# Kernel tuning notes

Measured on AMD Instinct MI355X. Metric: run time of the kernel, lower is better.

Reference implementation:

```python
import jax, jax.numpy as jnp
import numpy as np

B, N, D = 2, 4096, 256
H = 8
HD = D // H  # head dim = 32
DFF = 4 * D


def _layer_norm(x):
    # Matches source: (x - mean) / (std + 1e-6), std is population std (ddof=0)
    m = jnp.mean(x, axis=-1, keepdims=True)
    s = jnp.std(x, axis=-1, keepdims=True)
    return (x - m) / (s + 1e-6)


def setup_inputs() -> dict:
    key = jax.random.key(0)
    ks = jax.random.split(key, 11)
    sd = 1.0 / np.sqrt(D)
    sf = 1.0 / np.sqrt(DFF)
    return {
        "embeddings_in": jax.random.normal(ks[0], (B, N, D), dtype=jnp.float32),
        "Wq": jax.random.normal(ks[1], (D, D), dtype=jnp.float32) * sd,
        "bq": jnp.zeros((D,), dtype=jnp.float32),
        "Wk": jax.random.normal(ks[2], (D, D), dtype=jnp.float32) * sd,
        "bk": jnp.zeros((D,), dtype=jnp.float32),
        "Wv": jax.random.normal(ks[3], (D, D), dtype=jnp.float32) * sd,
        "bv": jnp.zeros((D,), dtype=jnp.float32),
        "Wo": jax.random.normal(ks[4], (D, D), dtype=jnp.float32) * sd,
        "bo": jnp.zeros((D,), dtype=jnp.float32),
        "W1": jax.random.normal(ks[5], (D, DFF), dtype=jnp.float32) * sd,
        "b1": jnp.zeros((DFF,), dtype=jnp.float32),
        "W2": jax.random.normal(ks[6], (DFF, D), dtype=jnp.float32) * sf,
        "b2": jnp.zeros((D,), dtype=jnp.float32),
    }


def reference(embeddings_in, Wq, bq, Wk, bk, Wv, bv, Wo, bo, W1, b1, W2, b2):
    x = embeddings_in
    xn1 = _layer_norm(x)
    # QKV projections, split into heads: [B,N,D] -> [B,H,N,HD]
    def heads(t):
        return jnp.transpose(t.reshape(B, N, H, HD), (0, 2, 1, 3))
    q = heads(xn1 @ Wq + bq)
    k = heads(xn1 @ Wk + bk)
    v = heads(xn1 @ Wv + bv)
    scores = jnp.einsum('bhnd,bhmd->bhnm', q, k) / jnp.sqrt(jnp.float32(HD))
    attn = jax.nn.softmax(scores, axis=-1)
    heads_out = jnp.einsum('bhnm,bhmd->bhnd', attn, v)
    attn_out = jnp.transpose(heads_out, (0, 2, 1, 3)).reshape(B, N, D)
    attn_out = attn_out @ Wo + bo  # dropout is identity in eval
    x_skip = attn_out + x
    xn2 = _layer_norm(x_skip)
    mlp = jax.nn.gelu(xn2 @ W1 + b1) @ W2 + b2
    return mlp + x_skip
```

## Files before the change

### kernel.cpp

```cpp
#include <hip/hip_runtime.h>
#include <hip/hip_bf16.h>

#define Bb 2
#define Nn 4096
#define Dd 256
#define Hh 8
#define HDh 32
#define DFFd 1024
#define MT (Bb*Nn)
#define Tt ((size_t)MT * Dd)
#define SPLIT 4
#define KVB (Nn / SPLIT)
#define NSTP (KVB / 64)

typedef __attribute__((ext_vector_type(8))) short short8;
typedef __attribute__((ext_vector_type(4))) float f32x4;
typedef __attribute__((address_space(1))) const unsigned int gu32;
typedef __attribute__((address_space(3))) unsigned int lu32;

__device__ __forceinline__ void gll16(const ushort* g, ushort* l) {
  __builtin_amdgcn_global_load_lds((gu32*)g, (lu32*)l, 16, 0, 0);
}
__device__ __forceinline__ float bf2f(ushort u){
  union { unsigned int i; float f; } v; v.i = ((unsigned int)u) << 16; return v.f;
}
__device__ __forceinline__ ushort f2bf(float f){
  union { float f; unsigned int i; } v; v.f = f;
  unsigned int r = v.i + 0x7fffu + ((v.i >> 16) & 1u);
  return (ushort)(r >> 16);
}
__device__ __forceinline__ int ars(int r){ return r * 64 + (r >> 3) * 32; }
__device__ __forceinline__ float gelu_f(float c){
  const float u = c * c;
  const float s = __builtin_fmaf(0.044715f * u, c, c);
  const float m = __builtin_amdgcn_exp2f(-2.302144404f * s);
  return c * __builtin_amdgcn_rcpf(1.0f + m);
}

__device__ __forceinline__ void ln_rows4(const float* __restrict__ x,
                                         ushort* __restrict__ out, int row0,
                                         int wave, int lane)
{
  #pragma unroll
  for (int r = 0; r < 4; r++) {
    const int row = row0 + wave * 4 + r;
    const float4 u = *(const float4*)(x + (size_t)row * Dd + lane * 4);
    float s1 = u.x + u.y + u.z + u.w;
    float s2 = u.x*u.x + u.y*u.y + u.z*u.z + u.w*u.w;
    #pragma unroll
    for (int m = 1; m < 64; m <<= 1) { s1 += __shfl_xor(s1, m, 64); s2 += __shfl_xor(s2, m, 64); }
    const float mean = s1 * (1.0f / Dd);
    float var = s2 * (1.0f / Dd) - mean * mean;
    var = var < 0.f ? 0.f : var;
    const float inv = 1.0f / (sqrtf(var) + 1e-6f);
    ushort4 o;
    o.x = f2bf((u.x - mean) * inv); o.y = f2bf((u.y - mean) * inv);
    o.z = f2bf((u.z - mean) * inv); o.w = f2bf((u.w - mean) * inv);
    *(ushort4*)(out + (size_t)row * Dd + lane * 4) = o;
  }
}

__global__ __launch_bounds__(256) void p0_kernel(
    const float* __restrict__ Wq, const float* __restrict__ Wk,
    const float* __restrict__ Wv, const float* __restrict__ Wo,
    const float* __restrict__ W1, const float* __restrict__ W2,
    const float* __restrict__ bq, const float* __restrict__ bk,
    const float* __restrict__ bv, ushort* __restrict__ wt,
    float* __restrict__ bqkv, const float* __restrict__ x,
    ushort* __restrict__ xn1)
{
  const int bid = blockIdx.x, t = threadIdx.x;
  __shared__ __align__(16) ushort T[64][72];
  if (bid < 192) {
    const float* src; ushort* dst; int Nsrc, Kdst, kt, nt;
    if (bid < 64) {
      const int m = bid >> 4, tile = bid & 15;
      kt = tile >> 2; nt = tile & 3; Nsrc = 256; Kdst = 256;
      src = (m == 0 ? Wq : m == 1 ? Wk : m == 2 ? Wv : Wo);
      dst = (m == 3) ? (wt + 196608) : (wt + m * 65536);
    } else if (bid < 128) {
      const int tile = bid - 64; kt = tile >> 4; nt = tile & 15;
      Nsrc = 1024; Kdst = 256; src = W1; dst = wt + 262144;
    } else {
      const int tile = bid - 128; kt = tile >> 2; nt = tile & 3;
      Nsrc = 256; Kdst = 1024; src = W2; dst = wt + 524288;
    }
    const int k0 = kt * 64, n0 = nt * 64;
    const int cc = t & 15, rr = t >> 4;
    #pragma unroll
    for (int pass = 0; pass < 4; pass++) {
      const int k = rr + pass * 16;
      const float4 v = *(const float4*)(src + (size_t)(k0 + k) * Nsrc + n0 + cc * 4);
      T[cc * 4 + 0][k] = f2bf(v.x); T[cc * 4 + 1][k] = f2bf(v.y);
      T[cc * 4 + 2][k] = f2bf(v.z); T[cc * 4 + 3][k] = f2bf(v.w);
    }
    __syncthreads();
    const int nl = t >> 2, ks = (t & 3) * 16;
    const short8 a = *(const short8*)(&T[nl][ks]);
    const short8 b = *(const short8*)(&T[nl][ks + 8]);
    ushort* drow = dst + (size_t)(n0 + nl) * Kdst + k0 + ks;
    *(short8*)(drow) = a; *(short8*)(drow + 8) = b;
  } else if (bid == 192) {
    bqkv[t] = bq[t]; bqkv[256 + t] = bk[t]; bqkv[512 + t] = bv[t];
  }
  ln_rows4(x, xn1, bid * 16, t >> 6, t & 63);
}

__global__ __launch_bounds__(256) void ln_kernel(const float* __restrict__ x,
                                                 ushort* __restrict__ out)
{
  ln_rows4(x, out, blockIdx.x * 16, threadIdx.x >> 6, threadIdx.x & 63);
}

template<int EPI>
__global__ __launch_bounds__(256) void gemm_wide(
    const ushort* __restrict__ A, const ushort* __restrict__ BT,
    const float* __restrict__ bias, void* __restrict__ outv, int N, int K)
{
  __shared__ __align__(16) ushort As[2][128 * 64];
  __shared__ __align__(16) ushort Bs[2][128 * 64];
  const int tid = threadIdx.x;
  const int wave = tid >> 6, lane = tid & 63;
  const int quad = lane >> 4, l15 = lane & 15;
  const int wm = wave >> 1, wn = wave & 1;
  const int n0 = blockIdx.x * 128, m0 = blockIdx.y * 128;
  f32x4 acc[4][4];
  #pragma unroll
  for (int mt = 0; mt < 4; mt++)
    #pragma unroll
    for (int nt = 0; nt < 4; nt++) acc[mt][nt] = (f32x4){0.f,0.f,0.f,0.f};
  const int srow = lane >> 3, scol = ((lane & 7) ^ srow) * 8;
  const ushort* gA[4];
  const ushort* gB[4];
  #pragma unroll
  for (int i = 0; i < 4; i++) {
    gA[i] = A  + (size_t)(m0 + i * 32 + wave * 8 + srow) * K + scol;
    gB[i] = BT + (size_t)(n0 + i * 32 + wave * 8 + srow) * K + scol;
  }
  int aoff[4], boff[4], cx[2];
  #pragma unroll
  for (int mt = 0; mt < 4; mt++) aoff[mt] = (wm * 64 + mt * 16 + l15) * 64;
  #pragma unroll
  for (int nt = 0; nt < 4; nt++) boff[nt] = (wn * 64 + nt * 16 + l15) * 64;
  #pragma unroll
  for (int kk = 0; kk < 2; kk++) cx[kk] = ((kk * 4 + quad) ^ (l15 & 7)) * 8;
  #pragma unroll
  for (int i = 0; i < 4; i++) {
    gll16(gA[i], &As[0][(i * 32 + wave * 8) * 64]);
    gll16(gB[i], &Bs[0][(i * 32 + wave * 8) * 64]);
  }
  __syncthreads();
  const int NC = K >> 6;
  int p = 0;
  for (int c = 0; c < NC; c++) {
    if (c + 1 < NC) {
      #pragma unroll
      for (int i = 0; i < 4; i++) {
        gll16(gA[i] + (c + 1) * 64, &As[p ^ 1][(i * 32 + wave * 8) * 64]);
        gll16(gB[i] + (c + 1) * 64, &Bs[p ^ 1][(i * 32 + wave * 8) * 64]);
      }
    }
    #pragma unroll
    for (int kk = 0; kk < 2; kk++) {
      short8 af[4];
      #pragma unroll
      for (int mt = 0; mt < 4; mt++)
        af[mt] = *(const short8*)(&As[p][aoff[mt] + cx[kk]]);
      #pragma unroll
      for (int nt = 0; nt < 4; nt++) {
        const short8 bf = *(const short8*)(&Bs[p][boff[nt] + cx[kk]]);
        #pragma unroll
        for (int mt = 0; mt < 4; mt++)
          acc[mt][nt] = __builtin_amdgcn_mfma_f32_16x16x32_bf16(af[mt], bf, acc[mt][nt], 0, 0, 0);
      }
    }
    __syncthreads();
    p ^= 1;
  }
  #pragma unroll
  for (int mt = 0; mt < 4; mt++) {
    const int row0 = m0 + wm * 64 + mt * 16 + quad * 4;
    #pragma unroll
    for (int nt = 0; nt < 4; nt++) {
      const int col = n0 + wn * 64 + nt * 16 + l15;
      const float bv = bias[col];
      float c[4];
      #pragma unroll
      for (int i = 0; i < 4; i++) c[i] = acc[mt][nt][i] + bv;
      if (EPI == 0) {
        ushort* qkv = (ushort*)outv;
        const int w = col >> 8, cd = col & 255;
        const int h = cd >> 5, hd = cd & 31;
        const int b = row0 >> 12, n = row0 & (Nn - 1);
        if (w < 2) {
          const float sc2 = (w == 0) ? (1.4426950408889634f * 0.17677669529663687f) : 1.0f;
          ushort* dst = qkv + (size_t)w * Tt + ((size_t)((b * Hh + h) * Nn) + n) * HDh + hd;
          #pragma unroll
          for (int i = 0; i < 4; i++) dst[(size_t)i * HDh] = f2bf(c[i] * sc2);
        } else {
          ushort4 pk;
          pk.x = f2bf(c[0]); pk.y = f2bf(c[1]); pk.z = f2bf(c[2]); pk.w = f2bf(c[3]);
          *(ushort4*)(qkv + 2 * Tt + ((size_t)((b * Hh + h) * HDh + hd)) * Nn + n) = pk;
        }
      } else {
        ushort* out = (ushort*)outv;
        #pragma unroll
        for (int i = 0; i < 4; i++)
          out[(size_t)(row0 + i) * N + col] = f2bf(gelu_f(c[i]));
      }
    }
  }
}

template<int EPI, int BM>
__global__ __launch_bounds__(256) void gemm_epi(
    const ushort* __restrict__ A, const ushort* __restrict__ BT,
    const float* __restrict__ bias, const float* __restrict__ res,
    void* __restrict__ outv, int N, int K)
{
  constexpr int MI = BM / 64;
  constexpr int AI = BM / 32;
  __shared__ __align__(16) ushort AsF[2][BM * 64 + (BM / 8) * 32];
  __shared__ __align__(16) ushort BsF[2][64 * 64 + 8 * 32];
  const int tid = threadIdx.x;
  const int wave = tid >> 6, lane = tid & 63;
  const int quad = lane >> 4, l15 = lane & 15;
  const int n0 = blockIdx.x * 64, m0 = blockIdx.y * BM;
  f32x4 acc[MI][4];
  #pragma unroll
  for (int mt = 0; mt < MI; mt++)
    #pragma unroll
    for (int nt = 0; nt < 4; nt++) acc[mt][nt] = (f32x4){0.f,0.f,0.f,0.f};
  const int srow = lane >> 3, scol = ((lane & 7) ^ srow) * 8;
  const ushort* gA[AI];
  #pragma unroll
  for (int ai = 0; ai < AI; ai++)
    gA[ai] = A + (size_t)(m0 + ai * 32 + wave * 8 + srow) * K + scol;
  const ushort* gB[2];
  #pragma unroll
  for (int bi = 0; bi < 2; bi++)
    gB[bi] = BT + (size_t)(n0 + bi * 32 + wave * 8 + srow) * K + scol;
  int aoff[MI], boff[4];
  #pragma unroll
  for (int mt = 0; mt < MI; mt++) aoff[mt] = ars(wave * 16 * MI + mt * 16 + l15);
  #pragma unroll
  for (int nt = 0; nt < 4; nt++) boff[nt] = ars(nt * 16 + l15);
  int cx[2];
  #pragma unroll
  for (int kk = 0; kk < 2; kk++) cx[kk] = ((kk * 4 + quad) ^ (l15 & 7)) * 8;
  #pragma unroll
  for (int ai = 0; ai < AI; ai++) gll16(gA[ai], &AsF[0][ars(ai * 32 + wave * 8)]);
  #pragma unroll
  for (int bi = 0; bi < 2; bi++) gll16(gB[bi], &BsF[0][ars(bi * 32 + wave * 8)]);
  __syncthreads();
  const int NC = K >> 6;
  int p = 0;
  for (int c = 0; c < NC; c++) {
    if (c + 1 < NC) {
      #pragma unroll
      for (int ai = 0; ai < AI; ai++)
        gll16(gA[ai] + (c + 1) * 64, &AsF[p ^ 1][ars(ai * 32 + wave * 8)]);
      #pragma unroll
      for (int bi = 0; bi < 2; bi++)
        gll16(gB[bi] + (c + 1) * 64, &BsF[p ^ 1][ars(bi * 32 + wave * 8)]);
    }
    #pragma unroll
    for (int kk = 0; kk < 2; kk++) {
      short8 af[MI];
      #pragma unroll
      for (int mt = 0; mt < MI; mt++)
        af[mt] = *(const short8*)(&AsF[p][aoff[mt] + cx[kk]]);
      #pragma unroll
      for (int nt = 0; nt < 4; nt++) {
        const short8 bf = *(const short8*)(&BsF[p][boff[nt] + cx[kk]]);
        #pragma unroll
        for (int mt = 0; mt < MI; mt++)
          acc[mt][nt] = __builtin_amdgcn_mfma_f32_16x16x32_bf16(af[mt], bf, acc[mt][nt], 0, 0, 0);
      }
    }
    __syncthreads();
    p ^= 1;
  }
  #pragma unroll
  for (int mt = 0; mt < MI; mt++) {
    const int row0 = m0 + wave * (16 * MI) + mt * 16 + quad * 4;
    #pragma unroll
    for (int nt = 0; nt < 4; nt++) {
      const int col = n0 + nt * 16 + l15;
      const float bv = bias[col];
      float c[4];
      #pragma unroll
      for (int i = 0; i < 4; i++) c[i] = acc[mt][nt][i] + bv;
      if (EPI == 1) {
        float* out = (float*)outv;
        #pragma unroll
        for (int i = 0; i < 4; i++) {
          const size_t idx = (size_t)(row0 + i) * N + col;
          out[idx] = c[i] + res[idx];
        }
      } else {
        ushort* out = (ushort*)outv;
        #pragma unroll
        for (int i = 0; i < 4; i++)
          out[(size_t)(row0 + i) * N + col] = f2bf(gelu_f(c[i]));
      }
    }
  }
}

__global__ __launch_bounds__(256, 4) void attn_kernel(
    const ushort* __restrict__ qp, const ushort* __restrict__ kp,
    const ushort* __restrict__ vtg, ushort* __restrict__ op0,
    ushort* __restrict__ op123, float* __restrict__ lp)
{
  __shared__ __align__(16) ushort Ks[2][64][32];
  __shared__ __align__(16) ushort Vt[2][32][72];
  __shared__ __align__(16) ushort Ps[4][64][40];
  const int tid = threadIdx.x;
  const int wave = tid >> 6, lane = tid & 63;
  const int quad = lane >> 4, l15 = lane & 15;
  const int qtb = blockIdx.x, bh = blockIdx.y, sp = blockIdx.z;
  const size_t base = (size_t)bh * Nn * HDh;
  const int q0 = qtb * 256 + wave * 64;
  short8 qf[4];
  #pragma unroll
  for (int qt = 0; qt < 4; qt++)
    qf[qt] = *(const short8*)(qp + base + (size_t)(q0 + qt * 16 + l15) * HDh + quad * 8);
  const int kv0 = sp * KVB;
  const ushort* kg = kp + base + (size_t)(kv0 + wave * 16 + (lane >> 2)) * HDh
                   + (((lane & 3) ^ ((lane >> 3) & 3)) * 8);
  const int kc = (quad ^ ((l15 >> 1) & 3)) * 8;
  const int vr = tid >> 3, vc = (tid & 7) * 8;
  const ushort* vg = vtg + base + (size_t)vr * Nn + kv0 + vc;
  ushort* psw = &Ps[wave][0][0];
  f32x4 o[2][4], ol[4];
  #pragma unroll
  for (int qt = 0; qt < 4; qt++) {
    o[0][qt] = (f32x4){0,0,0,0}; o[1][qt] = (f32x4){0,0,0,0};
    ol[qt] = (f32x4){0,0,0,0};
  }
  const short one = (short)0x3F80;
  const short8 ones = {one,one,one,one,one,one,one,one};
  const f32x4 zero4 = {0,0,0,0};
  const float SA = 8388608.0f;
  const float SB = 1065102389.0f;
  gll16(kg, &Ks[0][wave * 16][0]);
  int4 vreg = *(const int4*)vg;
  *(int4*)(&Vt[0][vr][vc]) = vreg;
  vreg = *(const int4*)(vg + 64);
  __syncthreads();
  #pragma unroll 2
  for (int step = 0; step < NSTP; step++) {
    const int p = step & 1;
    if (step + 1 < NSTP) {
      gll16(kg + (size_t)(step + 1) * 64 * HDh, &Ks[p ^ 1][wave * 16][0]);
      *(int4*)(&Vt[p ^ 1][vr][vc]) = vreg;
    }
    if (step + 2 < NSTP) vreg = *(const int4*)(vg + (size_t)(step + 2) * 64);
    #pragma unroll
    for (int half = 0; half < 2; half++) {
      #pragma unroll
      for (int nt2 = 0; nt2 < 2; nt2++) {
        const int nt = half * 2 + nt2;
        const short8 kf = *(const short8*)(&Ks[p][nt * 16 + l15][kc]);
        #pragma unroll
        for (int qt = 0; qt < 4; qt++) {
          const f32x4 s = __builtin_amdgcn_mfma_f32_16x16x32_bf16(kf, qf[qt], zero4, 0, 0, 0);
          const unsigned int i0 = (unsigned int)(int)fmaf(s[0], SA, SB);
          const unsigned int i1 = (unsigned int)(int)fmaf(s[1], SA, SB);
          const unsigned int i2 = (unsigned int)(int)fmaf(s[2], SA, SB);
          const unsigned int i3 = (unsigned int)(int)fmaf(s[3], SA, SB);
          uint2 pk;
          pk.x = __builtin_amdgcn_perm(i1, i0, 0x07060302u);
          pk.y = __builtin_amdgcn_perm(i3, i2, 0x07060302u);
          *(uint2*)(psw + (qt * 16 + l15) * 40 + nt2 * 16 + quad * 4) = pk;
        }
      }
      __builtin_amdgcn_wave_barrier();
      const short8 v0 = *(const short8*)(&Vt[p][l15][half * 32 + quad * 8]);
      const short8 v1 = *(const short8*)(&Vt[p][16 + l15][half * 32 + quad * 8]);
      #pragma unroll
      for (int qt = 0; qt < 4; qt++) {
        const short8 pb = *(const short8*)(psw + (qt * 16 + l15) * 40 + quad * 8);
        o[0][qt] = __builtin_amdgcn_mfma_f32_16x16x32_bf16(v0, pb, o[0][qt], 0, 0, 0);
        o[1][qt] = __builtin_amdgcn_mfma_f32_16x16x32_bf16(v1, pb, o[1][qt], 0, 0, 0);
        ol[qt]   = __builtin_amdgcn_mfma_f32_16x16x32_bf16(ones, pb, ol[qt], 0, 0, 0);
      }
      __builtin_amdgcn_wave_barrier();
    }
    __syncthreads();
  }
  lp[(size_t)sp * (16 * Nn) + (size_t)bh * Nn + q0 + lane] = ol[lane >> 4][0];
  ushort* ob = (sp == 0 ? op0 : op123 + (size_t)(sp - 1) * (16 * (size_t)Nn * HDh));
  #pragma unroll
  for (int pass = 0; pass < 2; pass++) {
    #pragma unroll
    for (int qt2 = 0; qt2 < 2; qt2++) {
      const int qt = pass * 2 + qt2;
      #pragma unroll
      for (int dt = 0; dt < 2; dt++) {
        ushort4 pk;
        pk.x = f2bf(o[dt][qt][0]); pk.y = f2bf(o[dt][qt][1]);
        pk.z = f2bf(o[dt][qt][2]); pk.w = f2bf(o[dt][qt][3]);
        *(ushort4*)(psw + (qt2 * 16 + l15) * 40 + dt * 16 + quad * 4) = pk;
      }
    }
    __builtin_amdgcn_wave_barrier();
    #pragma unroll
    for (int j = 0; j < 2; j++) {
      const int row = j * 16 + (lane >> 2);
      const short8 ov = *(const short8*)(psw + row * 40 + (lane & 3) * 8);
      const int q = q0 + pass * 32 + row;
      *(short8*)(ob + ((size_t)bh * Nn + q) * HDh + (lane & 3) * 8) = ov;
    }
    __builtin_amdgcn_wave_barrier();
  }
}

__global__ __launch_bounds__(256) void attn_combine(
    const ushort* __restrict__ op0, const ushort* __restrict__ op123,
    const float* __restrict__ lp, ushort* __restrict__ attn)
{
  const int idx = blockIdx.x * 256 + threadIdx.x;
  const int d8 = idx & 3, n = (idx >> 2) & (Nn - 1), bh = idx >> 14;
  const size_t ln = (size_t)bh * Nn + n;
  float l = 0.f;
  #pragma unroll
  for (int sp = 0; sp < SPLIT; sp++) l += lp[(size_t)sp * (16 * Nn) + ln];
  const float inv = 1.0f / l;
  float acc[8];
  #pragma unroll
  for (int k = 0; k < 8; k++) acc[k] = 0.f;
  const size_t qoff = ln * HDh + d8 * 8;
  #pragma unroll
  for (int sp = 0; sp < SPLIT; sp++) {
    const ushort* src = (sp == 0 ? op0 : op123 + (size_t)(sp - 1) * (16 * (size_t)Nn * HDh)) + qoff;
    const short8 u = *(const short8*)src;
    #pragma unroll
    for (int k = 0; k < 8; k++) acc[k] += bf2f((ushort)u[k]);
  }
  short8 ov;
  #pragma unroll
  for (int k = 0; k < 8; k++) ov[k] = (short)f2bf(acc[k] * inv);
  const int b = bh >> 3, h = bh & 7;
  *(short8*)(attn + ((size_t)(b * Nn + n)) * Dd + h * HDh + d8 * 8) = ov;
}

extern "C" void kernel_launch(void* const* d_in, const int* in_sizes, int n_in,
                              void* d_out, int out_size, void* d_ws, size_t ws_size,
                              hipStream_t stream)
{
  const float* x  = (const float*)d_in[0];
  const float* Wq = (const float*)d_in[1];
  const float* bq = (const float*)d_in[2];
  const float* Wk = (const float*)d_in[3];
  const float* bk = (const float*)d_in[4];
  const float* Wv = (const float*)d_in[5];
  const float* bv = (const float*)d_in[6];
  const float* Wo = (const float*)d_in[7];
  const float* bo = (const float*)d_in[8];
  const float* W1 = (const float*)d_in[9];
  const float* b1 = (const float*)d_in[10];
  const float* W2 = (const float*)d_in[11];
  const float* b2 = (const float*)d_in[12];

  char* ws = (char*)d_ws;
  ushort* wt    = (ushort*)ws;
  ushort* wtqkv = wt;
  ushort* wto   = wt + 196608;
  ushort* wt1   = wt + 262144;
  ushort* wt2   = wt + 524288;
  float*  bqkv  = (float*)(ws + 786432 * 2);
  ushort* s0    = (ushort*)(ws + 786432 * 2 + 4096);
  ushort* s1    = s0 + Tt;
  ushort* s2    = s1 + Tt;
  ushort* s3    = s2 + Tt;
  float*  xsk   = (float*)(s3 + Tt);
  ushort* xn2   = (ushort*)(xsk + Tt);
  ushort* xn1   = s0;
  ushort* hid   = s0;
  ushort* op0   = s0;
  ushort* op123 = (ushort*)xsk;
  float*  lp    = (float*)d_out;
  ushort* attnb = (ushort*)((char*)d_out + (4u << 20));
  float*  outp  = (float*)d_out;

  const dim3 blk(256);
  hipLaunchKernelGGL(p0_kernel, dim3(512), blk, 0, stream,
                     Wq, Wk, Wv, Wo, W1, W2, bq, bk, bv, wt, bqkv, x, xn1);
  hipLaunchKernelGGL((gemm_wide<0>), dim3(6, 64), blk, 0, stream,
                     xn1, wtqkv, bqkv, (void*)s1, 768, Dd);

  hipLaunchKernelGGL(attn_kernel, dim3(Nn / 256, Bb * Hh, SPLIT), blk, 0, stream,
                     s1, s2, s3, op0, op123, lp);
  hipLaunchKernelGGL(attn_combine, dim3((Bb * Hh * Nn * 4) / 256), blk, 0, stream,
                     op0, op123, lp, attnb);

  hipLaunchKernelGGL((gemm_epi<1,64>), dim3(4, 128), blk, 0, stream,
                     attnb, wto, bo, x, (void*)xsk, Dd, Dd);
  hipLaunchKernelGGL(ln_kernel, dim3(MT / 16), blk, 0, stream, xsk, xn2);
  hipLaunchKernelGGL((gemm_wide<2>), dim3(8, 64), blk, 0, stream,
                     xn2, wt1, b1, (void*)hid, DFFd, Dd);
  hipLaunchKernelGGL((gemm_epi<1,128>), dim3(4, 64), blk, 0, stream,
                     hid, wt2, b2, xsk, (void*)outp, Dd, DFFd);
}
```

Before: 189.4 us.

## Fuse attention split-combine, output projection, residual and LayerNorm into one kernel

Replaces the attn_combine, Wo GEMM and ln_kernel launches with a single wo_ln kernel. It merges the split-KV partial outputs while staging A tiles, runs the 256-wide Wo GEMM per 32-row block, and adds bias and the residual. It then computes the row LayerNorm in-register via shuffles and shared memory. This removes two launches and the round-trips of the combined attention tensor and xsk through global memory. The workspace is remapped so the hidden activation is split across two buffers, which needs extra pointer selection in the MLP GEMMs. The cost is a small per-block tile (grid of 256 blocks) with full Wo staged per block, which may reduce GEMM efficiency.

Measured after the change: 184.6 us. 1.03x faster.

```diff
diff --git a/kernel.cpp b/kernel.cpp
--- a/kernel.cpp
+++ b/kernel.cpp
@@ -106,16 +106,11 @@
   ln_rows4(x, xn1, bid * 16, t >> 6, t & 63);
 }
 
-__global__ __launch_bounds__(256) void ln_kernel(const float* __restrict__ x,
-                                                 ushort* __restrict__ out)
-{
-  ln_rows4(x, out, blockIdx.x * 16, threadIdx.x >> 6, threadIdx.x & 63);
-}
-
 template<int EPI>
 __global__ __launch_bounds__(256) void gemm_wide(
     const ushort* __restrict__ A, const ushort* __restrict__ BT,
-    const float* __restrict__ bias, void* __restrict__ outv, int N, int K)
+    const float* __restrict__ bias, void* __restrict__ outv, int N, int K,
+    void* __restrict__ outv2)
 {
   __shared__ __align__(16) ushort As[2][128 * 64];
   __shared__ __align__(16) ushort Bs[2][128 * 64];
@@ -203,18 +198,179 @@
           *(ushort4*)(qkv + 2 * Tt + ((size_t)((b * Hh + h) * HDh + hd)) * Nn + n) = pk;
         }
       } else {
-        ushort* out = (ushort*)outv;
+        ushort* ob = (m0 < 2048) ? (ushort*)outv
+                                 : (ushort*)outv2 - (size_t)2048 * N;
         #pragma unroll
         for (int i = 0; i < 4; i++)
-          out[(size_t)(row0 + i) * N + col] = f2bf(gelu_f(c[i]));
-      }
-    }
-  }
+          ob[(size_t)(row0 + i) * N + col] = f2bf(gelu_f(c[i]));
+      }
+    }
+  }
+}
+
+__global__ __launch_bounds__(256) void wo_ln(
+    const ushort* __restrict__ op0, const ushort* __restrict__ op123,
+    const float* __restrict__ lp, const ushort* __restrict__ BT,
+    const float* __restrict__ bo, const float* __restrict__ x,
+    float* __restrict__ xsk, ushort* __restrict__ xn2)
+{
+  __shared__ __align__(16) ushort As[2][32 * 64];
+  __shared__ __align__(16) ushort Bs[2][256 * 64];
+  __shared__ float Linv[32][8];
+  __shared__ float RS[2][4][32];
+  __shared__ float MN[32][2];
+  const int tid = threadIdx.x;
+  const int wave = tid >> 6, lane = tid & 63;
+  const int quad = lane >> 4, l15 = lane & 15;
+  const int m0 = blockIdx.x * 32;
+  const int srow = lane >> 3, scol = ((lane & 7) ^ srow) * 8;
+  int cx[2];
+  #pragma unroll
+  for (int kk = 0; kk < 2; kk++) cx[kk] = ((kk * 4 + quad) ^ (l15 & 7)) * 8;
+  const size_t SPS = (size_t)16 * Nn * HDh;
+  {
+    const int r = tid >> 3, h = tid & 7;
+    const int row = m0 + r;
+    const size_t li = (size_t)((row >> 12) * Hh + h) * Nn + (row & (Nn - 1));
+    float l = 0.f;
+    #pragma unroll
+    for (int sp = 0; sp < SPLIT; sp++) l += lp[sp * (16 * Nn) + li];
+    Linv[r][h] = 1.0f / l;
+  }
+  const int ar = tid >> 3, ae = tid & 7;
+  const int ah2 = ae >> 2, ahd0 = (ae & 3) * 8;
+  const int arow = m0 + ar;
+  const size_t abase = ((size_t)((arow >> 12) * Hh) * Nn + (arow & (Nn - 1))) * HDh + ahd0;
+  short8 a0, a1, a2, a3;
+  #define LOADA(cs) { \
+    const size_t off = abase + (size_t)((cs) * 2 + ah2) * (Nn * HDh); \
+    a0 = *(const short8*)(op0 + off); \
+    a1 = *(const short8*)(op123 + off); \
+    a2 = *(const short8*)(op123 + SPS + off); \
+    a3 = *(const short8*)(op123 + 2 * SPS + off); }
+  #define WRITEA(q, cs) { \
+    const float inv = Linv[ar][(cs) * 2 + ah2]; \
+    short8 w; \
+    _Pragma("unroll") \
+    for (int j = 0; j < 8; j++) { \
+      const float sum = ((bf2f((ushort)a0[j]) + bf2f((ushort)a1[j])) \
+                        + bf2f((ushort)a2[j])) + bf2f((ushort)a3[j]); \
+      w[j] = (short)f2bf(sum * inv); } \
+    *(short8*)(&As[q][ar * 64 + (ae ^ (ar & 7)) * 8]) = w; }
+  #define STAGEB(cs, q) { \
+    _Pragma("unroll") \
+    for (int i = 0; i < 8; i++) \
+      gll16(BT + (size_t)(wave * 64 + i * 8 + srow) * 256 + (cs) * 64 + scol, \
+            &Bs[q][(wave * 64 + i * 8) * 64]); }
+  LOADA(0);
+  STAGEB(0, 0);
+  __syncthreads();
+  WRITEA(0, 0);
+  __syncthreads();
+  f32x4 acc[2][4];
+  #pragma unroll
+  for (int mt = 0; mt < 2; mt++)
+    #pragma unroll
+    for (int nt = 0; nt < 4; nt++) acc[mt][nt] = (f32x4){0.f,0.f,0.f,0.f};
+  int p = 0;
+  #pragma unroll
+  for (int cs = 0; cs < 4; cs++) {
+    if (cs < 3) { LOADA(cs + 1); STAGEB(cs + 1, p ^ 1); }
+    #pragma unroll
+    for (int kk = 0; kk < 2; kk++) {
+      short8 af[2];
+      #pragma unroll
+      for (int mt = 0; mt < 2; mt++)
+        af[mt] = *(const short8*)(&As[p][(mt * 16 + l15) * 64 + cx[kk]]);
+      #pragma unroll
+      for (int nt = 0; nt < 4; nt++) {
+        const short8 bf = *(const short8*)(&Bs[p][(wave * 64 + nt * 16 + l15) * 64 + cx[kk]]);
+        #pragma unroll
+        for (int mt = 0; mt < 2; mt++)
+          acc[mt][nt] = __builtin_amdgcn_mfma_f32_16x16x32_bf16(af[mt], bf, acc[mt][nt], 0, 0, 0);
+      }
+    }
+    if (cs < 3) WRITEA(p ^ 1, cs + 1);
+    __syncthreads();
+    p ^= 1;
+  }
+  float v[2][4][4];
+  float s1[2][4], s2[2][4];
+  #pragma unroll
+  for (int mt = 0; mt < 2; mt++)
+    #pragma unroll
+    for (int i = 0; i < 4; i++) { s1[mt][i] = 0.f; s2[mt][i] = 0.f; }
+  #pragma unroll
+  for (int mt = 0; mt < 2; mt++) {
+    const int row0 = m0 + mt * 16 + quad * 4;
+    #pragma unroll
+    for (int nt = 0; nt < 4; nt++) {
+      const int col = wave * 64 + nt * 16 + l15;
+      const float bv = bo[col];
+      #pragma unroll
+      for (int i = 0; i < 4; i++) {
+        const size_t idx = (size_t)(row0 + i) * Dd + col;
+        const float t = (acc[mt][nt][i] + bv) + x[idx];
+        v[mt][nt][i] = t;
+        xsk[idx] = t;
+        s1[mt][i] += t;
+        s2[mt][i] += t * t;
+      }
+    }
+  }
+  #pragma unroll
+  for (int mt = 0; mt < 2; mt++)
+    #pragma unroll
+    for (int i = 0; i < 4; i++)
+      #pragma unroll
+      for (int m = 1; m < 16; m <<= 1) {
+        s1[mt][i] += __shfl_xor(s1[mt][i], m, 64);
+        s2[mt][i] += __shfl_xor(s2[mt][i], m, 64);
+      }
+  if (l15 == 0) {
+    #pragma unroll
+    for (int mt = 0; mt < 2; mt++)
+      #pragma unroll
+      for (int i = 0; i < 4; i++) {
+        const int r = mt * 16 + quad * 4 + i;
+        RS[0][wave][r] = s1[mt][i];
+        RS[1][wave][r] = s2[mt][i];
+      }
+  }
+  __syncthreads();
+  if (tid < 32) {
+    const float t1 = RS[0][0][tid] + RS[0][1][tid] + RS[0][2][tid] + RS[0][3][tid];
+    const float t2 = RS[1][0][tid] + RS[1][1][tid] + RS[1][2][tid] + RS[1][3][tid];
+    const float mean = t1 * (1.0f / Dd);
+    float var = t2 * (1.0f / Dd) - mean * mean;
+    var = var < 0.f ? 0.f : var;
+    MN[tid][0] = mean;
+    MN[tid][1] = 1.0f / (sqrtf(var) + 1e-6f);
+  }
+  __syncthreads();
+  #pragma unroll
+  for (int mt = 0; mt < 2; mt++) {
+    const int row0 = m0 + mt * 16 + quad * 4;
+    #pragma unroll
+    for (int i = 0; i < 4; i++) {
+      const int r = mt * 16 + quad * 4 + i;
+      const float mean = MN[r][0], inv = MN[r][1];
+      #pragma unroll
+      for (int nt = 0; nt < 4; nt++) {
+        const int col = wave * 64 + nt * 16 + l15;
+        xn2[(size_t)(row0 + i) * Dd + col] = f2bf((v[mt][nt][i] - mean) * inv);
+      }
+    }
+  }
+  #undef LOADA
+  #undef WRITEA
+  #undef STAGEB
 }
 
 template<int EPI, int BM>
 __global__ __launch_bounds__(256) void gemm_epi(
-    const ushort* __restrict__ A, const ushort* __restrict__ BT,
+    const ushort* __restrict__ A, const ushort* __restrict__ A2,
+    const ushort* __restrict__ BT,
     const float* __restrict__ bias, const float* __restrict__ res,
     void* __restrict__ outv, int N, int K)
 {
@@ -226,6 +382,7 @@
   const int wave = tid >> 6, lane = tid & 63;
   const int quad = lane >> 4, l15 = lane & 15;
   const int n0 = blockIdx.x * 64, m0 = blockIdx.y * BM;
+  const ushort* Abase = (m0 < 2048) ? A : A2 - (size_t)2048 * K;
   f32x4 acc[MI][4];
   #pragma unroll
   for (int mt = 0; mt < MI; mt++)
@@ -235,7 +392,7 @@
   const ushort* gA[AI];
   #pragma unroll
   for (int ai = 0; ai < AI; ai++)
-    gA[ai] = A + (size_t)(m0 + ai * 32 + wave * 8 + srow) * K + scol;
+    gA[ai] = Abase + (size_t)(m0 + ai * 32 + wave * 8 + srow) * K + scol;
   const ushort* gB[2];
   #pragma unroll
   for (int bi = 0; bi < 2; bi++)
@@ -415,35 +572,6 @@
     }
     __builtin_amdgcn_wave_barrier();
   }
-}
-
-__global__ __launch_bounds__(256) void attn_combine(
-    const ushort* __restrict__ op0, const ushort* __restrict__ op123,
-    const float* __restrict__ lp, ushort* __restrict__ attn)
-{
-  const int idx = blockIdx.x * 256 + threadIdx.x;
-  const int d8 = idx & 3, n = (idx >> 2) & (Nn - 1), bh = idx >> 14;
-  const size_t ln = (size_t)bh * Nn + n;
-  float l = 0.f;
-  #pragma unroll
-  for (int sp = 0; sp < SPLIT; sp++) l += lp[(size_t)sp * (16 * Nn) + ln];
-  const float inv = 1.0f / l;
-  float acc[8];
-  #pragma unroll
-  for (int k = 0; k < 8; k++) acc[k] = 0.f;
-  const size_t qoff = ln * HDh + d8 * 8;
-  #pragma unroll
-  for (int sp = 0; sp < SPLIT; sp++) {
-    const ushort* src = (sp == 0 ? op0 : op123 + (size_t)(sp - 1) * (16 * (size_t)Nn * HDh)) + qoff;
-    const short8 u = *(const short8*)src;
-    #pragma unroll
-    for (int k = 0; k < 8; k++) acc[k] += bf2f((ushort)u[k]);
-  }
-  short8 ov;
-  #pragma unroll
-  for (int k = 0; k < 8; k++) ov[k] = (short)f2bf(acc[k] * inv);
-  const int b = bh >> 3, h = bh & 7;
-  *(short8*)(attn + ((size_t)(b * Nn + n)) * Dd + h * HDh + d8 * 8) = ov;
 }
 
 extern "C" void kernel_launch(void* const* d_in, const int* in_sizes, int n_in,
@@ -475,32 +603,31 @@
   ushort* s1    = s0 + Tt;
   ushort* s2    = s1 + Tt;
   ushort* s3    = s2 + Tt;
-  float*  xsk   = (float*)(s3 + Tt);
-  ushort* xn2   = (ushort*)(xsk + Tt);
+  ushort* oxsk  = s3 + Tt;
   ushort* xn1   = s0;
-  ushort* hid   = s0;
   ushort* op0   = s0;
-  ushort* op123 = (ushort*)xsk;
+  ushort* op123 = oxsk;
+  float*  xskN  = (float*)s1;
+  ushort* xn2N  = s3;
+  ushort* hid1  = s0;
+  ushort* hid2  = oxsk;
   float*  lp    = (float*)d_out;
-  ushort* attnb = (ushort*)((char*)d_out + (4u << 20));
   float*  outp  = (float*)d_out;
 
   const dim3 blk(256);
   hipLaunchKernelGGL(p0_kernel, dim3(512), blk, 0, stream,
                      Wq, Wk, Wv, Wo, W1, W2, bq, bk, bv, wt, bqkv, x, xn1);
   hipLaunchKernelGGL((gemm_wide<0>), dim3(6, 64), blk, 0, stream,
-                     xn1, wtqkv, bqkv, (void*)s1, 768, Dd);
+                     xn1, wtqkv, bqkv, (void*)s1, 768, Dd, (void*)nullptr);
 
   hipLaunchKernelGGL(attn_kernel, dim3(Nn / 256, Bb * Hh, SPLIT), blk, 0, stream,
                      s1, s2, s3, op0, op123, lp);
-  hipLaunchKernelGGL(attn_combine, dim3((Bb * Hh * Nn * 4) / 256), blk, 0, stream,
-                     op0, op123, lp, attnb);
-
-  hipLaunchKernelGGL((gemm_epi<1,64>), dim3(4, 128), blk, 0, stream,
-                     attnb, wto, bo, x, (void*)xsk, Dd, Dd);
-  hipLaunchKernelGGL(ln_kernel, dim3(MT / 16), blk, 0, stream, xsk, xn2);
+
+  hipLaunchKernelGGL(wo_ln, dim3(MT / 32), blk, 0, stream,
+                     op0, op123, lp, wto, bo, x, xskN, xn2N);
+
   hipLaunchKernelGGL((gemm_wide<2>), dim3(8, 64), blk, 0, stream,
-                     xn2, wt1, b1, (void*)hid, DFFd, Dd);
+                     xn2N, wt1, b1, (void*)hid1, DFFd, Dd, (void*)hid2);
   hipLaunchKernelGGL((gemm_epi<1,128>), dim3(4, 64), blk, 0, stream,
-                     hid, wt2, b2, xsk, (void*)outp, Dd, DFFd);
-}
+                     hid1, hid2, wt2, b2, xskN, (void*)outp, Dd, DFFd);
+}
```
